# Optimization experiments

Measured on AMD Instinct MI355X. Metric: run time of the kernel, lower is better.

## Reference

```python
import jax, jax.numpy as jnp
import numpy as np

H = 512; W = 512; C_IN = 14; HID = 128; N_CELLS = 8192

def _rn(k, shape, sc=0.05):
    return jax.random.normal(k, shape, jnp.float32) * sc

def setup_inputs() -> dict:
    key = jax.random.key(0)
    ks = jax.random.split(key, 32)
    inp = {
        'x': jax.random.normal(ks[0], (1, C_IN, H, W), jnp.float32),
        'cell_i': jax.random.randint(ks[1], (N_CELLS,), 0, H, jnp.int32),
        'cell_j': jax.random.randint(ks[2], (N_CELLS,), 0, W, jnp.int32),
        'action': jax.random.randint(ks[3], (N_CELLS, 4), 0, 2, jnp.int32),
        'w1': _rn(ks[4], (48, C_IN, 3, 3)), 'b1': _rn(ks[5], (48,)),
        'g1': jnp.ones((48,), jnp.float32), 'be1': jnp.zeros((48,), jnp.float32),
        'w2': _rn(ks[6], (96, 48, 3, 3)), 'b2': _rn(ks[7], (96,)),
        'g2': jnp.ones((96,), jnp.float32), 'be2': jnp.zeros((96,), jnp.float32),
        'w3': _rn(ks[8], (HID, 96, 3, 3)), 'b3': _rn(ks[9], (HID,)),
        'g3': jnp.ones((HID,), jnp.float32), 'be3': jnp.zeros((HID,), jnp.float32),
        'fw1': _rn(ks[10], (HID * 9, 256)), 'fb1': _rn(ks[11], (256,)),
        'fw2': _rn(ks[12], (256, 128)), 'fb2': _rn(ks[13], (128,)),
        'bw': _rn(ks[14], (128, 4)), 'bb': _rn(ks[15], (4,)),
        'iw': _rn(ks[16], (128, 4)), 'ib': _rn(ks[17], (4,)),
        'tw': _rn(ks[18], (128, 4)), 'tb': _rn(ks[19], (4,)),
        'vw1': _rn(ks[20], (HID, 64)), 'vb1': _rn(ks[21], (64,)),
        'vw2': _rn(ks[22], (64, 1)), 'vb2': _rn(ks[23], (1,)),
    }
    return inp

def _conv(x, w, b):
    y = jax.lax.conv_general_dilated(x, w, (1, 1), 'SAME',
                                     dimension_numbers=('NCHW', 'OIHW', 'NCHW'))
    return y + b[None, :, None, None]

def _gn(x, gamma, beta, groups, eps=1e-5):
    n, c, h, w = x.shape
    xr = x.reshape(n, groups, -1)
    m = xr.mean(axis=2, keepdims=True)
    v = xr.var(axis=2, keepdims=True)
    xn = ((xr - m) * jax.lax.rsqrt(v + eps)).reshape(n, c, h, w)
    return xn * gamma[None, :, None, None] + beta[None, :, None, None]

def _forward(x, cell_i, cell_j, action, w1, b1, g1, be1, w2, b2, g2, be2,
             w3, b3, g3, be3, fw1, fb1, fw2, fb2, bw, bb, iw, ib, tw, tb,
             vw1, vb1, vw2, vb2):
    # Encoder: conv -> GN -> ReLU x3
    f = jax.nn.relu(_gn(_conv(x, w1, b1), g1, be1, 6))
    f = jax.nn.relu(_gn(_conv(f, w2, b2), g2, be2, 12))
    f = jax.nn.relu(_gn(_conv(f, w3, b3), g3, be3, 16))  # (1, HID, H, W)
    # Value head: global avg pool -> MLP
    pooled = f.mean(axis=(2, 3))  # (1, HID)
    value = jax.nn.relu(pooled @ vw1 + vb1) @ vw2 + vb2  # (1, 1)
    # Per-burning-cell 3x3 patch gather (zero-padded borders)
    fpad = jnp.pad(f, ((0, 0), (0, 0), (1, 1), (1, 1)))[0]  # (HID, H+2, W+2)
    def slice_patch(i, j):
        return jax.lax.dynamic_slice(fpad, (0, i, j), (HID, 3, 3))
    patches = jax.vmap(slice_patch)(cell_i, cell_j)  # (N, HID, 3, 3)
    flat = patches.reshape(patches.shape[0], HID * 9)
    shared = jax.nn.relu(jax.nn.relu(flat @ fw1 + fb1) @ fw2 + fb2)  # (N, 128)
    burn_logits = shared @ bw + bb
    intensity = shared @ iw + ib
    temp = shared @ tw + tb
    p = jnp.clip(jax.nn.sigmoid(burn_logits), 1e-7, 1.0 - 1e-7)
    a = action.astype(jnp.float32)
    log_prob = jnp.sum(a * jnp.log(p) + (1.0 - a) * jnp.log(1.0 - p))
    entropy = -jnp.sum(p * jnp.log(p) + (1.0 - p) * jnp.log(1.0 - p))
    # Scatter sampled actions into grid at N/E/S/W neighbors (in-bounds only)
    di = jnp.array([-1, 0, 1, 0], jnp.int32)
    dj = jnp.array([0, 1, 0, -1], jnp.int32)
    ni = cell_i[:, None] + di
    nj = cell_j[:, None] + dj
    valid = (ni >= 0) & (ni < H) & (nj >= 0) & (nj < W) & (a > 0.5)
    grid = jnp.zeros((H, W), jnp.float32).at[
        jnp.clip(ni, 0, H - 1), jnp.clip(nj, 0, W - 1)].max(valid.astype(jnp.float32))
    return grid, log_prob, entropy, value, intensity, temp

def reference(x, cell_i, cell_j, action, w1, b1, g1, be1, w2, b2, g2, be2,
              w3, b3, g3, be3, fw1, fb1, fw2, fb2, bw, bb, iw, ib, tw, tb,
              vw1, vb1, vw2, vb2):
    return _forward(x, cell_i, cell_j, action, w1, b1, g1, be1, w2, b2, g2, be2,
                    w3, b3, g3, be3, fw1, fb1, fw2, fb2, bw, bb, iw, ib, tw, tb,
                    vw1, vb1, vw2, vb2)
```

## Files before the change

### kernel.cpp

```cpp
#include <hip/hip_runtime.h>
#include <hip/hip_bf16.h>
#include <cstddef>

#define NPIX 262144
#define PW 514
typedef __hip_bfloat16 bf16;
typedef __attribute__((ext_vector_type(8))) short short8;
typedef __attribute__((ext_vector_type(4))) float f32x4;

__device__ inline unsigned short f2bfu(float f){
  __hip_bfloat16 h = __float2bfloat16(f);
  return *(reinterpret_cast<unsigned short*>(&h));
}
__device__ inline float bflo(unsigned u){ return __uint_as_float(u<<16); }
__device__ inline float bfhi(unsigned u){ return __uint_as_float(u & 0xffff0000u); }
__device__ inline unsigned pack2bf(float a, float b){
  unsigned ua = __float_as_uint(a), ub = __float_as_uint(b);
  return ((ua + 0x8000u) >> 16) | ((ub + 0x8000u) & 0xffff0000u);
}
__device__ inline void dma16(const bf16* g, unsigned short* l){
  __builtin_amdgcn_global_load_lds(
      (const __attribute__((address_space(1))) unsigned int*)g,
      (__attribute__((address_space(3))) unsigned int*)l, 16, 0, 0);
}

__device__ inline void computeAB(const float* stats, const float* gamma, const float* beta,
                                 int c, float& A, float& B){
  int g = c >> 3;
  const float invN = 1.f/2097152.f;
  float m = stats[g*2]*invN;
  float v = stats[g*2+1]*invN - m*m;
  float inv = rsqrtf(v + 1e-5f);
  A = inv*gamma[c];
  B = beta[c] - m*A;
}

__global__ void setup_kernel(float* out, float* stats, float* pooled,
                             const float* __restrict__ w1, bf16* __restrict__ wT1,
                             const float* __restrict__ w2, bf16* __restrict__ wT2,
                             const float* __restrict__ w3, bf16* __restrict__ wT3,
                             const float* __restrict__ fw1, bf16* __restrict__ wF1T,
                             const float* __restrict__ fw2, bf16* __restrict__ wF2T){
  int b = blockIdx.x;
  if (b < 1025){
    int i = b*256 + threadIdx.x;
    if (i < 262147) out[i] = 0.f;
    if (i < 68)  stats[i]  = 0.f;
    if (i < 128) pooled[i] = 0.f;
    return;
  }
  b -= 1025;
  if (b < 30){
    int idx = b*256 + threadIdx.x;
    if (idx < 5*48*32){
      int kp = idx & 31; int oc = (idx >> 5) % 48; int kc = idx / (48*32);
      int k = kc*32 + kp;
      int tap = k >> 4, c = k & 15;
      float v = (tap < 9 && c < 14) ? w1[(oc*14 + c)*9 + tap] : 0.f;
      wT1[idx] = __float2bfloat16(v);
    }
    return;
  }
  b -= 30;
  if (b < 216){
    int idx = b*256 + threadIdx.x;
    if (idx < 9*2*96*32){
      int cp = idx & 31; int rest = idx >> 5;
      int oc = rest % 96; rest /= 96;
      int cc = rest % 2; int tap = rest / 2;
      int ic = cc*32 + cp;
      float v = (ic < 48) ? w2[(oc*48 + ic)*9 + tap] : 0.f;
      wT2[idx] = __float2bfloat16(v);
    }
    return;
  }
  b -= 216;
  if (b < 432){
    int idx = b*256 + threadIdx.x;
    if (idx < 9*3*128*32){
      int cp = idx & 31; int rest = idx >> 5;
      int oc = rest & 127; rest >>= 7;
      int cc = rest % 3; int tap = rest / 3;
      int ic = cc*32 + cp;
      float v = (ic < 96) ? w3[(oc*96 + ic)*9 + tap] : 0.f;
      wT3[idx] = __float2bfloat16(v);
    }
    return;
  }
  b -= 432;
  if (b < 1152){
    int idx = b*256 + threadIdx.x;
    if (idx < 36*256*32){
      int kp = idx & 31; int oc = (idx >> 5) & 255; int kc = idx >> 13;
      int k2 = kc*32 + kp;
      int rr = k2 >> 7, ch = k2 & 127;
      wF1T[idx] = __float2bfloat16(fw1[(size_t)(ch*9 + rr)*256 + oc]);
    }
    return;
  }
  b -= 1152;
  {
    int idx = b*256 + threadIdx.x;
    if (idx < 8*128*32){
      int kp = idx & 31; int oc = (idx >> 5) & 127; int kc = idx >> 12;
      wF2T[idx] = __float2bfloat16(fw2[(size_t)(kc*32 + kp)*128 + oc]);
    }
  }
}

__launch_bounds__(256,2)
__global__ void conv1_mfma_kernel(const float* __restrict__ x, const bf16* __restrict__ wT,
                                  const float* __restrict__ bias, bf16* __restrict__ out,
                                  float* __restrict__ stats){
  constexpr int XP = 24;
  __shared__ unsigned short sX[324*XP];
  __shared__ float sStat[96];
  const int tid = threadIdx.x;
  const int lane = tid & 63, wave = tid >> 6;
  const int quad = lane >> 4, l15 = lane & 15;
  const int tileX = (blockIdx.x & 31)*16, tileY = (blockIdx.x >> 5)*16;
  if (tid < 96) sStat[tid] = 0.f;
  for (int p = tid; p < 324; p += 256){ sX[p*XP+14] = 0; sX[p*XP+15] = 0; }
  for (int idx = tid; idx < 14*324; idx += 256){
    int c = idx / 324, p = idx - c*324;
    int r = p / 18, col = p - r*18;
    int gy = tileY + r - 1, gx = tileX + col - 1;
    float v = 0.f;
    if ((unsigned)gy < 512u && (unsigned)gx < 512u) v = x[(size_t)c*NPIX + gy*512 + gx];
    sX[p*XP + c] = f2bfu(v);
  }
  __syncthreads();

  f32x4 acc[3][4];
  #pragma unroll
  for (int t = 0; t < 3; ++t){
    f32x4 bv = *(const f32x4*)(bias + t*16 + quad*4);
    #pragma unroll
    for (int s = 0; s < 4; ++s) acc[t][s] = bv;
  }
  const int pxb = wave*4;
  const int h = quad >> 1, chalf = (quad & 1)*8;
  const int T0[5] = {0,2,4,6,8};
  const int T1[5] = {1,3,5,7,8};
  #pragma unroll
  for (int kc = 0; kc < 5; ++kc){
    short8 a[3];
    #pragma unroll
    for (int t = 0; t < 3; ++t)
      a[t] = *(const short8*)((const unsigned short*)wT + (size_t)(kc*48 + t*16 + l15)*32 + quad*8);
    const int ky = h ? (T1[kc]/3) : (T0[kc]/3);
    const int kx = h ? (T1[kc]%3) : (T0[kc]%3);
    #pragma unroll
    for (int s = 0; s < 4; ++s){
      int py = pxb + s;
      short8 bfr = *(const short8*)(&sX[((py+ky)*18 + l15+kx)*XP + chalf]);
      #pragma unroll
      for (int t = 0; t < 3; ++t)
        acc[t][s] = __builtin_amdgcn_mfma_f32_16x16x32_bf16(a[t], bfr, acc[t][s], 0, 0, 0);
    }
  }
  #pragma unroll
  for (int t = 0; t < 3; ++t){
    #pragma unroll
    for (int r = 0; r < 4; ++r){
      float sv = 0.f, sq = 0.f;
      #pragma unroll
      for (int s = 0; s < 4; ++s){ float v = acc[t][s][r]; sv += v; sq += v*v; }
      #pragma unroll
      for (int m = 1; m < 16; m <<= 1){ sv += __shfl_xor(sv, m); sq += __shfl_xor(sq, m); }
      if (l15 == 0){
        atomicAdd(&sStat[(t*16 + quad*4 + r)*2],   sv);
        atomicAdd(&sStat[(t*16 + quad*4 + r)*2+1], sq);
      }
    }
    #pragma unroll
    for (int s = 0; s < 4; ++s){
      f32x4 v = acc[t][s];
      uint2 pk;
      pk.x = pack2bf(v[0], v[1]);
      pk.y = pack2bf(v[2], v[3]);
      *(uint2*)(out + ((size_t)(tileY+pxb+s+1)*PW + tileX+l15+1)*48 + t*16 + quad*4) = pk;
    }
  }
  __syncthreads();
  if (tid < 12){
    int g = tid >> 1, wsel = tid & 1;
    float v = 0.f;
    #pragma unroll
    for (int j = 0; j < 8; ++j) v += sStat[(g*8+j)*2 + wsel];
    atomicAdd(&stats[g*2 + wsel], v);
  }
}

template<int C>
__global__ void norm_kernel(bf16* buf, const float* __restrict__ stats,
                            const float* __restrict__ gamma, const float* __restrict__ beta){
  __shared__ float sAB[2*C];
  const int tid = threadIdx.x;
  if (tid < C){ float A,B; computeAB(stats, gamma, beta, tid, A, B); sAB[tid]=A; sAB[C+tid]=B; }
  __syncthreads();
  const int y = blockIdx.x >> 2, q = blockIdx.x & 3;
  uint4* row = (uint4*)(buf + (size_t)y*PW*C);
  constexpr int NU4 = PW*C/8/4;
  const bool brow = (y == 0) | (y == 513);
  for (int i = q*NU4 + tid; i < (q+1)*NU4; i += 256){
    int e = i*8;
    int px = e / C;
    if (brow | (px == 0) | (px == 513)){ row[i] = make_uint4(0,0,0,0); continue; }
    int ch = e - px*C;
    uint4 v = row[i];
    unsigned uu[4] = {v.x,v.y,v.z,v.w}, ou[4];
    #pragma unroll
    for (int j = 0; j < 4; ++j){
      float a = fmaxf(bflo(uu[j])*sAB[ch+j*2]   + sAB[C+ch+j*2],   0.f);
      float d = fmaxf(bfhi(uu[j])*sAB[ch+j*2+1] + sAB[C+ch+j*2+1], 0.f);
      ou[j] = pack2bf(a, d);
    }
    row[i] = make_uint4(ou[0],ou[1],ou[2],ou[3]);
  }
}

template<int IC, int NCC, int OCT, int OC>
__launch_bounds__(256, 2)
__global__ void conv_dma16_kernel(const bf16* __restrict__ in, const bf16* __restrict__ wT,
                                  const float* __restrict__ bias,
                                  bf16* __restrict__ out, float* __restrict__ outstats){
  __shared__ unsigned short sIn[2][1296*8];
  __shared__ float sStat[2*OC];
  const int tid  = threadIdx.x;
  const int lane = tid & 63, wave = tid >> 6;
  const int quad = lane >> 4, l15 = lane & 15;
  const int ocg = wave >> 1, pxg = wave & 1;
  const int tileX = (blockIdx.x & 31) * 16, tileY = (blockIdx.x >> 5) * 16;
  const int ocbase = ocg * (OCT*16);

  for (int i = tid; i < 2*OC; i += 256) sStat[i] = 0.f;

  unsigned off[6];
  #pragma unroll
  for (int k = 0; k < 6; ++k){
    int slot = tid + k*256;
    if (k < 5 || tid < 16){
      int row = slot/72; int rem = slot - row*72;
      int cc = rem/18;   int col = rem - cc*18;
      off[k] = (unsigned)(((tileY+row)*PW + tileX+col)*IC + cc*8);
    }
  }
  auto issueDMA = [&](int cr, int bi){
    #pragma unroll
    for (int k = 0; k < 6; ++k){
      if (k == 5 && tid >= 16) continue;
      dma16(in + off[k] + cr*32, &sIn[bi][(tid + k*256)*8]);
    }
  };

  f32x4 acc[OCT][8];
  #pragma unroll
  for (int t = 0; t < OCT; ++t){
    f32x4 bv = *(const f32x4*)(bias + ocbase + t*16 + quad*4);
    #pragma unroll
    for (int s = 0; s < 8; ++s) acc[t][s] = bv;
  }

  issueDMA(0, 0);
  __syncthreads();

  #pragma unroll 1
  for (int cr = 0; cr < NCC; ++cr){
    const unsigned short* B0 = &sIn[cr & 1][(((pxg*8)*4 + quad)*18 + l15)*8];
    const unsigned short* W0 = (const unsigned short*)wT + ((size_t)cr*OC + ocbase + l15)*32 + quad*8;

    #pragma unroll
    for (int tap = 0; tap < 9; ++tap){
      if (tap == 7 && cr + 1 < NCC) issueDMA(cr + 1, (cr + 1) & 1);
      const int ky = tap/3, kx = tap - ky*3;
      short8 a[OCT];
      #pragma unroll
      for (int t = 0; t < OCT; ++t)
        a[t] = *(const short8*)(W0 + (size_t)tap*(NCC*OC*32) + t*512);
      #pragma unroll
      for (int s = 0; s < 8; ++s){
        short8 b = *(const short8*)(B0 + ((s+ky)*72 + kx)*8);
        #pragma unroll
        for (int t = 0; t < OCT; ++t)
          acc[t][s] = __builtin_amdgcn_mfma_f32_16x16x32_bf16(a[t], b, acc[t][s], 0, 0, 0);
      }
    }
    __syncthreads();
  }

  #pragma unroll
  for (int t = 0; t < OCT; ++t){
    #pragma unroll
    for (int r = 0; r < 4; ++r){
      float sv = 0.f, sq = 0.f;
      #pragma unroll
      for (int s = 0; s < 8; ++s){ float v = acc[t][s][r]; sv += v; sq += v*v; }
      #pragma unroll
      for (int m = 1; m < 16; m <<= 1){ sv += __shfl_xor(sv, m); sq += __shfl_xor(sq, m); }
      if (l15 == 0){
        atomicAdd(&sStat[(ocbase + t*16 + quad*4 + r)*2],   sv);
        atomicAdd(&sStat[(ocbase + t*16 + quad*4 + r)*2+1], sq);
      }
    }
    #pragma unroll
    for (int s = 0; s < 8; ++s){
      int py = pxg*8 + s;
      f32x4 v = acc[t][s];
      uint2 pk;
      pk.x = pack2bf(v[0], v[1]);
      pk.y = pack2bf(v[2], v[3]);
      *(uint2*)(out + ((size_t)(tileY+py+1)*PW + (tileX+l15+1))*OC + ocbase + t*16 + quad*4) = pk;
    }
  }
  __syncthreads();
  if (tid < (OC/8)*2){
    int g = tid >> 1, wsel = tid & 1;
    float v = 0.f;
    #pragma unroll
    for (int j = 0; j < 8; ++j) v += sStat[(g*8+j)*2 + wsel];
    atomicAdd(&outstats[g*2 + wsel], v);
  }
}

template<int IC, int NCC, int OCT, int OC, int NW, int TH>
__launch_bounds__(NW*64, 3)
__global__ void conv_dma8_kernel(const bf16* __restrict__ in, const bf16* __restrict__ wT,
                                 const float* __restrict__ bias,
                                 bf16* __restrict__ out, float* __restrict__ outstats){
  constexpr int NT   = NW*64;
  constexpr int ROWS = TH + 2;
  constexpr int SLOTS = ROWS * 72;
  constexpr int K    = (SLOTS + NT - 1) / NT;
  constexpr int REM  = SLOTS - (K-1)*NT;
  __shared__ unsigned short sIn[2][SLOTS*8];
  __shared__ float sStat[2*OC];
  const int tid  = threadIdx.x;
  const int lane = tid & 63, wave = tid >> 6;
  const int quad = lane >> 4, l15 = lane & 15;
  const int tileX = (blockIdx.x & 31) * 16, tileY = (blockIdx.x >> 5) * TH;
  const int ocbase = wave * (OCT*16);

  for (int i = tid; i < 2*OC; i += NT) sStat[i] = 0.f;

  unsigned off[K];
  #pragma unroll
  for (int k = 0; k < K; ++k){
    int slot = tid + k*NT;
    if (k < K-1 || tid < REM){
      int row = slot/72; int rem = slot - row*72;
      int cc = rem/18;   int col = rem - cc*18;
      off[k] = (unsigned)(((tileY+row)*PW + tileX+col)*IC + cc*8);
    }
  }
  auto issueDMA = [&](int cr, int bi){
    #pragma unroll
    for (int k = 0; k < K; ++k){
      if (k == K-1 && tid >= REM) continue;
      dma16(in + off[k] + cr*32, &sIn[bi][(tid + k*NT)*8]);
    }
  };

  f32x4 acc[OCT][TH];
  #pragma unroll
  for (int t = 0; t < OCT; ++t){
    f32x4 bv = *(const f32x4*)(bias + ocbase + t*16 + quad*4);
    #pragma unroll
    for (int s = 0; s < TH; ++s) acc[t][s] = bv;
  }

  issueDMA(0, 0);
  __syncthreads();

  #pragma unroll 1
  for (int cr = 0; cr < NCC; ++cr){
    if (cr + 1 < NCC) issueDMA(cr + 1, (cr + 1) & 1);
    const unsigned short* B0 = &sIn[cr & 1][(quad*18 + l15)*8];
    const unsigned short* W0 = (const unsigned short*)wT + ((size_t)cr*OC + ocbase + l15)*32 + quad*8;

    #pragma unroll
    for (int kx = 0; kx < 3; ++kx){
      short8 a[3][OCT];
      #pragma unroll
      for (int ky = 0; ky < 3; ++ky)
        #pragma unroll
        for (int t = 0; t < OCT; ++t)
          a[ky][t] = *(const short8*)(W0 + (size_t)(ky*3+kx)*(NCC*OC*32) + t*512);
      #pragma unroll
      for (int r = 0; r < ROWS; ++r){
        short8 b = *(const short8*)(B0 + (r*72 + kx)*8);
        #pragma unroll
        for (int ky = 0; ky < 3; ++ky){
          const int s = r - ky;
          if (s >= 0 && s < TH){
            #pragma unroll
            for (int t = 0; t < OCT; ++t)
              acc[t][s] = __builtin_amdgcn_mfma_f32_16x16x32_bf16(a[ky][t], b, acc[t][s], 0, 0, 0);
          }
        }
      }
    }
    __syncthreads();
  }

  #pragma unroll
  for (int t = 0; t < OCT; ++t){
    #pragma unroll
    for (int r = 0; r < 4; ++r){
      float sv = 0.f, sq = 0.f;
      #pragma unroll
      for (int s = 0; s < TH; ++s){ float v = acc[t][s][r]; sv += v; sq += v*v; }
      #pragma unroll
      for (int m = 1; m < 16; m <<= 1){ sv += __shfl_xor(sv, m); sq += __shfl_xor(sq, m); }
      if (l15 == 0){
        atomicAdd(&sStat[(ocbase + t*16 + quad*4 + r)*2],   sv);
        atomicAdd(&sStat[(ocbase + t*16 + quad*4 + r)*2+1], sq);
      }
    }
    #pragma unroll
    for (int s = 0; s < TH; ++s){
      f32x4 v = acc[t][s];
      uint2 pk;
      pk.x = pack2bf(v[0], v[1]);
      pk.y = pack2bf(v[2], v[3]);
      *(uint2*)(out + ((size_t)(tileY+s+1)*PW + (tileX+l15+1))*OC + ocbase + t*16 + quad*4) = pk;
    }
  }
  __syncthreads();
  if (tid < (OC/8)*2){
    int g = tid >> 1, wsel = tid & 1;
    float v = 0.f;
    #pragma unroll
    for (int j = 0; j < 8; ++j) v += sStat[(g*8+j)*2 + wsel];
    atomicAdd(&outstats[g*2 + wsel], v);
  }
}

__launch_bounds__(256)
__global__ void mega_kernel(const bf16* __restrict__ f, const float* __restrict__ instats,
                            const float* __restrict__ gamma, const float* __restrict__ beta,
                            const int* __restrict__ cell_i, const int* __restrict__ cell_j,
                            const int* __restrict__ action,
                            const bf16* __restrict__ wT, const float* __restrict__ fb1,
                            const bf16* __restrict__ wT2, const float* __restrict__ fb2,
                            const float* __restrict__ bw, const float* __restrict__ bb,
                            const float* __restrict__ iw, const float* __restrict__ ib,
                            const float* __restrict__ tw, const float* __restrict__ tb,
                            float* __restrict__ pooled, float* __restrict__ out){
  constexpr int KST = 1160;
  __shared__ unsigned short sG[16*KST];
  __shared__ unsigned short h1L[16*264];
  __shared__ float sAB[256];
  __shared__ int sij[32];
  __shared__ float sRed[2];
  __shared__ float sP[128];
  float* h2L = (float*)sG;
  const int tid = threadIdx.x;
  const int lane = tid & 63, wave = tid >> 6;
  const int quad = lane >> 4, l15 = lane & 15;
  const int cb = blockIdx.x*16;

  if (tid < 2) sRed[tid] = 0.f;
  if (tid < 128){ float A,B; computeAB(instats, gamma, beta, tid, A, B);
    sAB[tid]=A; sAB[128+tid]=B; sP[tid]=0.f; }
  if (tid < 16) sij[tid] = cell_i[cb + tid];
  else if (tid < 32) sij[tid] = cell_j[cb + tid - 16];
  __syncthreads();

  for (int idx = tid; idx < 16*144; idx += 256){
    int c8 = idx & 15; int t2 = idx >> 4;
    int cell = t2 / 9, rr = t2 - cell*9;
    int r = rr/3, cl = rr - r*3;
    int py = sij[cell] + r, px = sij[16+cell] + cl;
    uint4 v = *(const uint4*)(f + ((size_t)py*PW + px)*128 + c8*8);
    bool border = (py==0) | (py==513) | (px==0) | (px==513);
    unsigned uu[4] = {v.x, v.y, v.z, v.w};
    unsigned ou[4];
    #pragma unroll
    for (int j = 0; j < 4; ++j){
      int ch = c8*8 + j*2;
      float a = border ? 0.f : fmaxf(bflo(uu[j])*sAB[ch]   + sAB[128+ch],   0.f);
      float d = border ? 0.f : fmaxf(bfhi(uu[j])*sAB[ch+1] + sAB[128+ch+1], 0.f);
      ou[j] = pack2bf(a, d);
    }
    uint4 wv; wv.x = ou[0]; wv.y = ou[1]; wv.z = ou[2]; wv.w = ou[3];
    *(uint4*)(&sG[cell*KST + rr*128 + c8*8]) = wv;
  }
  __syncthreads();

  {
    f32x4 acc[4];
    const int ocb = wave*64;
    #pragma unroll
    for (int t = 0; t < 4; ++t)
      acc[t] = *(const f32x4*)(fb1 + ocb + t*16 + quad*4);
    #pragma unroll 2
    for (int kc = 0; kc < 36; ++kc){
      short8 b = *(const short8*)(&sG[l15*KST + kc*32 + quad*8]);
      #pragma unroll
      for (int t = 0; t < 4; ++t){
        short8 a = *(const short8*)((const unsigned short*)wT + ((size_t)kc*256 + ocb + t*16 + l15)*32 + quad*8);
        acc[t] = __builtin_amdgcn_mfma_f32_16x16x32_bf16(a, b, acc[t], 0, 0, 0);
      }
    }
    #pragma unroll
    for (int t = 0; t < 4; ++t){
      f32x4 v = acc[t];
      uint2 pk;
      pk.x = pack2bf(fmaxf(v[0],0.f), fmaxf(v[1],0.f));
      pk.y = pack2bf(fmaxf(v[2],0.f), fmaxf(v[3],0.f));
      *(uint2*)(&h1L[l15*264 + ocb + t*16 + quad*4]) = pk;
    }
  }
  __syncthreads();

  {
    const int och = wave*32;
    f32x4 acc2[2];
    #pragma unroll
    for (int t = 0; t < 2; ++t)
      acc2[t] = *(const f32x4*)(fb2 + och + t*16 + quad*4);
    #pragma unroll
    for (int kc = 0; kc < 8; ++kc){
      short8 b = *(const short8*)(&h1L[l15*264 + kc*32 + quad*8]);
      #pragma unroll
      for (int t = 0; t < 2; ++t){
        short8 a = *(const short8*)((const unsigned short*)wT2 + ((size_t)kc*128 + och + t*16 + l15)*32 + quad*8);
        acc2[t] = __builtin_amdgcn_mfma_f32_16x16x32_bf16(a, b, acc2[t], 0, 0, 0);
      }
    }
    #pragma unroll
    for (int t = 0; t < 2; ++t){
      f32x4 v = acc2[t];
      #pragma unroll
      for (int r = 0; r < 4; ++r) v[r] = fmaxf(v[r], 0.f);
      *(f32x4*)(&h2L[l15*132 + och + t*16 + quad*4]) = v;
    }
  }
  __syncthreads();

  if (tid < 192){
    int cell = tid/12, jj = tid - cell*12;
    int which = jj >> 2, o = jj & 3;
    const float* W  = (which==0) ? bw : (which==1 ? iw : tw);
    const float* Bp = (which==0) ? bb : (which==1 ? ib : tb);
    float d = Bp[o];
    const float* h2 = &h2L[cell*132];
    for (int k = 0; k < 128; k++) d += h2[k]*W[k*4+o];
    int cellg = cb + cell;
    if (which == 1){
      out[262147 + cellg*4 + o] = d;
    } else if (which == 2){
      out[262147 + 32768 + cellg*4 + o] = d;
    } else {
      float p = 1.f/(1.f + __expf(-d));
      p = fminf(fmaxf(p, 1e-7f), 1.f - 1e-7f);
      int a = action[cellg*4 + o];
      float lp  = a ? __logf(p) : __logf(1.f-p);
      float ent = -(p*__logf(p) + (1.f-p)*__logf(1.f-p));
      atomicAdd(&sRed[0], lp);
      atomicAdd(&sRed[1], ent);
      if (a){
        const int di[4] = {-1,0,1,0};
        const int dj[4] = {0,1,0,-1};
        int ni = sij[cell] + di[o];
        int nj = sij[16+cell] + dj[o];
        if ((unsigned)ni < 512u && (unsigned)nj < 512u)
          out[ni*512 + nj] = 1.0f;
      }
    }
  }

  {
    const int gl = tid & 15, xl = tid >> 4;
    float A[8], B[8];
    #pragma unroll
    for (int j = 0; j < 8; ++j){ A[j] = sAB[gl*8+j]; B[j] = sAB[128+gl*8+j]; }
    const int y = blockIdx.x;
    float ps[8] = {0,0,0,0,0,0,0,0};
    for (int x2 = xl; x2 < 512; x2 += 16){
      uint4 v = *(const uint4*)(f + ((size_t)(y+1)*PW + x2+1)*128 + gl*8);
      unsigned uu[4] = {v.x, v.y, v.z, v.w};
      #pragma unroll
      for (int j = 0; j < 4; ++j){
        ps[j*2]   += fmaxf(bflo(uu[j])*A[j*2]   + B[j*2],   0.f);
        ps[j*2+1] += fmaxf(bfhi(uu[j])*A[j*2+1] + B[j*2+1], 0.f);
      }
    }
    #pragma unroll
    for (int j = 0; j < 8; ++j) atomicAdd(&sP[gl*8+j], ps[j]);
  }
  __syncthreads();
  if (tid == 0){
    atomicAdd(&out[262144], sRed[0]);
    atomicAdd(&out[262145], sRed[1]);
  }
  if (tid < 128) atomicAdd(&pooled[tid], sP[tid]);
}

__global__ void value_kernel(const float* __restrict__ pooled, const float* __restrict__ vw1,
                             const float* __restrict__ vb1, const float* __restrict__ vw2,
                             const float* __restrict__ vb2, float* __restrict__ out){
  int t = threadIdx.x;
  float h = vb1[t];
  const float invN = 1.f/262144.f;
  for (int c = 0; c < 128; c++) h += (pooled[c]*invN)*vw1[c*64+t];
  h = fmaxf(h, 0.f);
  float v = h*vw2[t];
  #pragma unroll
  for (int off = 32; off; off >>= 1) v += __shfl_xor(v, off);
  if (t == 0) out[262146] = v + vb2[0];
}

extern "C" void kernel_launch(void* const* d_in, const int* in_sizes, int n_in,
                              void* d_out, int out_size, void* d_ws, size_t ws_size,
                              hipStream_t stream) {
  (void)in_sizes; (void)n_in; (void)out_size; (void)ws_size;
  const float* x      = (const float*)d_in[0];
  const int*  cell_i  = (const int*)d_in[1];
  const int*  cell_j  = (const int*)d_in[2];
  const int*  action  = (const int*)d_in[3];
  const float* w1 = (const float*)d_in[4];  const float* b1 = (const float*)d_in[5];
  const float* g1 = (const float*)d_in[6];  const float* be1= (const float*)d_in[7];
  const float* w2 = (const float*)d_in[8];  const float* b2 = (const float*)d_in[9];
  const float* g2 = (const float*)d_in[10]; const float* be2= (const float*)d_in[11];
  const float* w3 = (const float*)d_in[12]; const float* b3 = (const float*)d_in[13];
  const float* g3 = (const float*)d_in[14]; const float* be3= (const float*)d_in[15];
  const float* fw1= (const float*)d_in[16]; const float* fb1= (const float*)d_in[17];
  const float* fw2= (const float*)d_in[18]; const float* fb2= (const float*)d_in[19];
  const float* bw = (const float*)d_in[20]; const float* bb = (const float*)d_in[21];
  const float* iw = (const float*)d_in[22]; const float* ib = (const float*)d_in[23];
  const float* tw = (const float*)d_in[24]; const float* tb = (const float*)d_in[25];
  const float* vw1= (const float*)d_in[26]; const float* vb1= (const float*)d_in[27];
  const float* vw2= (const float*)d_in[28]; const float* vb2= (const float*)d_in[29];

  float* out = (float*)d_out;
  char* ws = (char*)d_ws;
  bf16* buf1 = (bf16*)(ws);
  bf16* buf2 = (bf16*)(ws + 25362816);
  bf16* bufF = (bf16*)(ws + 76088448);
  bf16* wT2  = (bf16*)(ws + 143722624);
  bf16* wT3  = (bf16*)(ws + 143833216);
  bf16* wT1  = (bf16*)(ws + 144054400);
  bf16* wF1T = (bf16*)(ws + 144069760);
  bf16* wF2T = (bf16*)(ws + 144659584);
  float* statsf = (float*)(ws + 144725120);
  float* pooled = statsf + 128;

  setup_kernel<<<2983, 256, 0, stream>>>(out, statsf, pooled, w1, wT1, w2, wT2, w3, wT3,
                                         fw1, wF1T, fw2, wF2T);
  conv1_mfma_kernel<<<1024, 256, 0, stream>>>(x, wT1, b1, buf1, statsf + 0);
  norm_kernel<48><<<514*4, 256, 0, stream>>>(buf1, statsf + 0, g1, be1);
  conv_dma16_kernel<48,2,3,96><<<1024, 256, 0, stream>>>(buf1, wT2, b2, buf2, statsf + 12);
  norm_kernel<96><<<514*4, 256, 0, stream>>>(buf2, statsf + 12, g2, be2);
  conv_dma8_kernel<96,3,2,128,4,8><<<2048, 256, 0, stream>>>(buf2, wT3, b3, bufF, statsf + 36);
  mega_kernel<<<512, 256, 0, stream>>>(bufF, statsf + 36, g3, be3, cell_i, cell_j, action,
                                       wF1T, fb1, wF2T, fb2, bw, bb, iw, ib, tw, tb,
                                       pooled, out);
  value_kernel<<<1, 64, 0, stream>>>(pooled, vw1, vb1, vw2, vb2, out);
}
```

Baseline: 353.2 us.

## Fuse GroupNorm+ReLU into conv2/conv3 LDS tiles and drop norm kernels

Removes the two standalone norm_kernel passes, which read and rewrote the full padded activation buffers in place. The GroupNorm scale/shift and ReLU are now applied in LDS right after each DMA'd input chunk lands, and border pixels are zeroed there instead of in memory. Conv3 moves to one LDS buffer per channel chunk, and both convs use an explicitly staged DMA/transform/compute sequence in place of the loop. This saves two launches and a large amount of global memory traffic. In exchange, halo pixels are transformed redundantly, LDS use grows, and extra barriers may serialize part of the compute.

```diff
diff --git a/kernel.cpp b/kernel.cpp
--- a/kernel.cpp
+++ b/kernel.cpp
@@ -33,6 +33,20 @@
   float inv = rsqrtf(v + 1e-5f);
   A = inv*gamma[c];
   B = beta[c] - m*A;
+}
+
+__device__ inline uint4 gnrelu16(uint4 v, const float* __restrict__ ab, bool border){
+  unsigned uu[4] = {v.x, v.y, v.z, v.w};
+  unsigned ou[4];
+  #pragma unroll
+  for (int j = 0; j < 4; ++j){
+    f32x4 abv = *(const f32x4*)(ab + j*4);
+    float a = fmaxf(bflo(uu[j])*abv[0] + abv[1], 0.f);
+    float d = fmaxf(bfhi(uu[j])*abv[2] + abv[3], 0.f);
+    ou[j] = pack2bf(a, d);
+  }
+  if (border) return make_uint4(0u,0u,0u,0u);
+  return make_uint4(ou[0], ou[1], ou[2], ou[3]);
 }
 
 __global__ void setup_kernel(float* out, float* stats, float* pooled,
@@ -192,41 +206,17 @@
   }
 }
 
-template<int C>
-__global__ void norm_kernel(bf16* buf, const float* __restrict__ stats,
-                            const float* __restrict__ gamma, const float* __restrict__ beta){
-  __shared__ float sAB[2*C];
-  const int tid = threadIdx.x;
-  if (tid < C){ float A,B; computeAB(stats, gamma, beta, tid, A, B); sAB[tid]=A; sAB[C+tid]=B; }
-  __syncthreads();
-  const int y = blockIdx.x >> 2, q = blockIdx.x & 3;
-  uint4* row = (uint4*)(buf + (size_t)y*PW*C);
-  constexpr int NU4 = PW*C/8/4;
-  const bool brow = (y == 0) | (y == 513);
-  for (int i = q*NU4 + tid; i < (q+1)*NU4; i += 256){
-    int e = i*8;
-    int px = e / C;
-    if (brow | (px == 0) | (px == 513)){ row[i] = make_uint4(0,0,0,0); continue; }
-    int ch = e - px*C;
-    uint4 v = row[i];
-    unsigned uu[4] = {v.x,v.y,v.z,v.w}, ou[4];
-    #pragma unroll
-    for (int j = 0; j < 4; ++j){
-      float a = fmaxf(bflo(uu[j])*sAB[ch+j*2]   + sAB[C+ch+j*2],   0.f);
-      float d = fmaxf(bfhi(uu[j])*sAB[ch+j*2+1] + sAB[C+ch+j*2+1], 0.f);
-      ou[j] = pack2bf(a, d);
-    }
-    row[i] = make_uint4(ou[0],ou[1],ou[2],ou[3]);
-  }
-}
-
 template<int IC, int NCC, int OCT, int OC>
 __launch_bounds__(256, 2)
 __global__ void conv_dma16_kernel(const bf16* __restrict__ in, const bf16* __restrict__ wT,
                                   const float* __restrict__ bias,
+                                  const float* __restrict__ instats,
+                                  const float* __restrict__ gamma, const float* __restrict__ beta,
                                   bf16* __restrict__ out, float* __restrict__ outstats){
+  constexpr int CPAD = NCC*32;
   __shared__ unsigned short sIn[2][1296*8];
   __shared__ float sStat[2*OC];
+  __shared__ __align__(16) float sAB2[2*CPAD];
   const int tid  = threadIdx.x;
   const int lane = tid & 63, wave = tid >> 6;
   const int quad = lane >> 4, l15 = lane & 15;
@@ -235,15 +225,23 @@
   const int ocbase = ocg * (OCT*16);
 
   for (int i = tid; i < 2*OC; i += 256) sStat[i] = 0.f;
-
-  unsigned off[6];
+  for (int c = tid; c < CPAD; c += 256){
+    float A = 0.f, B = 0.f;
+    if (c < IC) computeAB(instats, gamma, beta, c, A, B);
+    sAB2[2*c] = A; sAB2[2*c+1] = B;
+  }
+
+  unsigned off[6]; int cbk[6]; bool bfk[6];
   #pragma unroll
   for (int k = 0; k < 6; ++k){
     int slot = tid + k*256;
     if (k < 5 || tid < 16){
       int row = slot/72; int rem = slot - row*72;
       int cc = rem/18;   int col = rem - cc*18;
-      off[k] = (unsigned)(((tileY+row)*PW + tileX+col)*IC + cc*8);
+      int py = tileY + row, px = tileX + col;
+      off[k] = (unsigned)((py*PW + px)*IC + cc*8);
+      cbk[k] = cc*16;
+      bfk[k] = (py==0) | (py==513) | (px==0) | (px==513);
     }
   }
   auto issueDMA = [&](int cr, int bi){
@@ -253,6 +251,14 @@
       dma16(in + off[k] + cr*32, &sIn[bi][(tid + k*256)*8]);
     }
   };
+  auto transformLDS = [&](int cr, int bi){
+    #pragma unroll
+    for (int k = 0; k < 6; ++k){
+      if (k == 5 && tid >= 16) continue;
+      uint4* p = (uint4*)&sIn[bi][(tid + k*256)*8];
+      *p = gnrelu16(*p, &sAB2[cbk[k] + cr*64], bfk[k]);
+    }
+  };
 
   f32x4 acc[OCT][8];
   #pragma unroll
@@ -262,17 +268,11 @@
     for (int s = 0; s < 8; ++s) acc[t][s] = bv;
   }
 
-  issueDMA(0, 0);
-  __syncthreads();
-
-  #pragma unroll 1
-  for (int cr = 0; cr < NCC; ++cr){
-    const unsigned short* B0 = &sIn[cr & 1][(((pxg*8)*4 + quad)*18 + l15)*8];
+  auto computeChunk = [&](int cr, int bi){
+    const unsigned short* B0 = &sIn[bi][(((pxg*8)*4 + quad)*18 + l15)*8];
     const unsigned short* W0 = (const unsigned short*)wT + ((size_t)cr*OC + ocbase + l15)*32 + quad*8;
-
     #pragma unroll
     for (int tap = 0; tap < 9; ++tap){
-      if (tap == 7 && cr + 1 < NCC) issueDMA(cr + 1, (cr + 1) & 1);
       const int ky = tap/3, kx = tap - ky*3;
       short8 a[OCT];
       #pragma unroll
@@ -286,8 +286,17 @@
           acc[t][s] = __builtin_amdgcn_mfma_f32_16x16x32_bf16(a[t], b, acc[t][s], 0, 0, 0);
       }
     }
-    __syncthreads();
-  }
+  };
+
+  issueDMA(0, 0);
+  __syncthreads();
+  issueDMA(1, 1);
+  transformLDS(0, 0);
+  __syncthreads();
+  transformLDS(1, 1);
+  computeChunk(0, 0);
+  __syncthreads();
+  computeChunk(1, 1);
 
   #pragma unroll
   for (int t = 0; t < OCT; ++t){
@@ -327,14 +336,19 @@
 __launch_bounds__(NW*64, 3)
 __global__ void conv_dma8_kernel(const bf16* __restrict__ in, const bf16* __restrict__ wT,
                                  const float* __restrict__ bias,
+                                 const float* __restrict__ instats,
+                                 const float* __restrict__ gamma, const float* __restrict__ beta,
                                  bf16* __restrict__ out, float* __restrict__ outstats){
   constexpr int NT   = NW*64;
   constexpr int ROWS = TH + 2;
   constexpr int SLOTS = ROWS * 72;
   constexpr int K    = (SLOTS + NT - 1) / NT;
   constexpr int REM  = SLOTS - (K-1)*NT;
-  __shared__ unsigned short sIn[2][SLOTS*8];
+  constexpr int CPAD = NCC*32;
+  static_assert(NCC == 3, "conv3 path");
+  __shared__ unsigned short sIn[NCC][SLOTS*8];
   __shared__ float sStat[2*OC];
+  __shared__ __align__(16) float sAB2[2*CPAD];
   const int tid  = threadIdx.x;
   const int lane = tid & 63, wave = tid >> 6;
   const int quad = lane >> 4, l15 = lane & 15;
@@ -342,22 +356,38 @@
   const int ocbase = wave * (OCT*16);
 
   for (int i = tid; i < 2*OC; i += NT) sStat[i] = 0.f;
-
-  unsigned off[K];
+  for (int c = tid; c < CPAD; c += NT){
+    float A = 0.f, B = 0.f;
+    if (c < IC) computeAB(instats, gamma, beta, c, A, B);
+    sAB2[2*c] = A; sAB2[2*c+1] = B;
+  }
+
+  unsigned off[K]; int cbk[K]; bool bfk[K];
   #pragma unroll
   for (int k = 0; k < K; ++k){
     int slot = tid + k*NT;
     if (k < K-1 || tid < REM){
       int row = slot/72; int rem = slot - row*72;
       int cc = rem/18;   int col = rem - cc*18;
-      off[k] = (unsigned)(((tileY+row)*PW + tileX+col)*IC + cc*8);
-    }
-  }
-  auto issueDMA = [&](int cr, int bi){
+      int py = tileY + row, px = tileX + col;
+      off[k] = (unsigned)((py*PW + px)*IC + cc*8);
+      cbk[k] = cc*16;
+      bfk[k] = (py==0) | (py==513) | (px==0) | (px==513);
+    }
+  }
+  auto issueDMA = [&](int cr){
     #pragma unroll
     for (int k = 0; k < K; ++k){
       if (k == K-1 && tid >= REM) continue;
-      dma16(in + off[k] + cr*32, &sIn[bi][(tid + k*NT)*8]);
+      dma16(in + off[k] + cr*32, &sIn[cr][(tid + k*NT)*8]);
+    }
+  };
+  auto transformLDS = [&](int cr){
+    #pragma unroll
+    for (int k = 0; k < K; ++k){
+      if (k == K-1 && tid >= REM) continue;
+      uint4* p = (uint4*)&sIn[cr][(tid + k*NT)*8];
+      *p = gnrelu16(*p, &sAB2[cbk[k] + cr*64], bfk[k]);
     }
   };
 
@@ -369,15 +399,9 @@
     for (int s = 0; s < TH; ++s) acc[t][s] = bv;
   }
 
-  issueDMA(0, 0);
-  __syncthreads();
-
-  #pragma unroll 1
-  for (int cr = 0; cr < NCC; ++cr){
-    if (cr + 1 < NCC) issueDMA(cr + 1, (cr + 1) & 1);
-    const unsigned short* B0 = &sIn[cr & 1][(quad*18 + l15)*8];
+  auto computeChunk = [&](int cr){
+    const unsigned short* B0 = &sIn[cr][(quad*18 + l15)*8];
     const unsigned short* W0 = (const unsigned short*)wT + ((size_t)cr*OC + ocbase + l15)*32 + quad*8;
-
     #pragma unroll
     for (int kx = 0; kx < 3; ++kx){
       short8 a[3][OCT];
@@ -400,8 +424,21 @@
         }
       }
     }
-    __syncthreads();
-  }
+  };
+
+  issueDMA(0);
+  __syncthreads();
+  issueDMA(1);
+  transformLDS(0);
+  __syncthreads();
+  issueDMA(2);
+  transformLDS(1);
+  computeChunk(0);
+  __syncthreads();
+  transformLDS(2);
+  computeChunk(1);
+  __syncthreads();
+  computeChunk(2);
 
   #pragma unroll
   for (int t = 0; t < OCT; ++t){
@@ -650,10 +687,10 @@
   setup_kernel<<<2983, 256, 0, stream>>>(out, statsf, pooled, w1, wT1, w2, wT2, w3, wT3,
                                          fw1, wF1T, fw2, wF2T);
   conv1_mfma_kernel<<<1024, 256, 0, stream>>>(x, wT1, b1, buf1, statsf + 0);
-  norm_kernel<48><<<514*4, 256, 0, stream>>>(buf1, statsf + 0, g1, be1);
-  conv_dma16_kernel<48,2,3,96><<<1024, 256, 0, stream>>>(buf1, wT2, b2, buf2, statsf + 12);
-  norm_kernel<96><<<514*4, 256, 0, stream>>>(buf2, statsf + 12, g2, be2);
-  conv_dma8_kernel<96,3,2,128,4,8><<<2048, 256, 0, stream>>>(buf2, wT3, b3, bufF, statsf + 36);
+  conv_dma16_kernel<48,2,3,96><<<1024, 256, 0, stream>>>(buf1, wT2, b2, statsf + 0, g1, be1,
+                                                         buf2, statsf + 12);
+  conv_dma8_kernel<96,3,2,128,4,8><<<2048, 256, 0, stream>>>(buf2, wT3, b3, statsf + 12, g2, be2,
+                                                             bufF, statsf + 36);
   mega_kernel<<<512, 256, 0, stream>>>(bufF, statsf + 36, g3, be3, cell_i, cell_j, action,
                                        wF1T, fb1, wF2T, fb2, bw, bb, iw, ib, tw, tb,
                                        pooled, out);
```

After: 398.2 us. 1.13x slower.
